# Optimization experiments

Hardware: AMD Instinct MI355X
Metric: run time of the kernel (lower is better)

## Reference

```python
import jax, jax.numpy as jnp
import numpy as np

B, S, D, H = 2, 2048, 1024, 16
HD = D // H

def setup_inputs() -> dict:
    key = jax.random.key(0)
    ks = jax.random.split(key, 5)
    s = 1.0 / np.sqrt(D)
    return {
        "x": jax.random.normal(ks[0], (B, S, D), dtype=jnp.float32),
        "Wq": jax.random.normal(ks[1], (D, D), dtype=jnp.float32) * s,
        "Wk": jax.random.normal(ks[2], (D, D), dtype=jnp.float32) * s,
        "Wv": jax.random.normal(ks[3], (D, D), dtype=jnp.float32) * s,
        "Wo": jax.random.normal(ks[4], (D, D), dtype=jnp.float32) * s,
        "bo": jnp.zeros((D,), dtype=jnp.float32),
    }

def reference(x, Wq, Wk, Wv, Wo, bo):
    b, n, _ = x.shape
    # QKV projections (no bias), reshape to [B, H, S, HD]
    def proj(W):
        return (x @ W.T).reshape(b, n, H, HD).transpose(0, 2, 1, 3)
    q, k, v = proj(Wq), proj(Wk), proj(Wv)
    scores = jnp.einsum("bhqd,bhkd->bhqk", q, k)
    causal = jnp.triu(jnp.ones((n, n), dtype=bool), k=1)
    scores = jnp.where(causal, -jnp.inf, scores)
    attn = jax.nn.softmax(scores / np.sqrt(HD), axis=-1)  # dropout p=0.0 (eval)
    ctx = jnp.einsum("bhqk,bhkd->bhqd", attn, v)
    ctx = ctx.transpose(0, 2, 1, 3).reshape(b, n, D)
    return ctx @ Wo.T + bo
```

## Files before the change

### kernel.cpp

```cpp
#include <hip/hip_runtime.h>
#include <stdint.h>


typedef __bf16 bf16_t;
typedef __bf16 bf16x8 __attribute__((ext_vector_type(8)));
typedef float  f32x4  __attribute__((ext_vector_type(4)));
typedef uint32_t u32x4 __attribute__((ext_vector_type(4)));

#define MFMA16(A, B, C) __builtin_amdgcn_mfma_f32_16x16x32_bf16(A, B, C, 0, 0, 0)

__device__ __forceinline__ void async_ld16(const bf16_t* g, bf16_t* l) {
  __builtin_amdgcn_global_load_lds(
      (const __attribute__((address_space(1))) void*)g,
      (__attribute__((address_space(3))) void*)l, 16, 0, 0);
}

__device__ __forceinline__ u32x4 ld8(const float* p) {
  const float4 a = *(const float4*)p;
  const float4 b = *(const float4*)(p + 4);
  union { u32x4 v; bf16_t h[8]; } r;
  r.h[0] = (bf16_t)a.x; r.h[1] = (bf16_t)a.y;
  r.h[2] = (bf16_t)a.z; r.h[3] = (bf16_t)a.w;
  r.h[4] = (bf16_t)b.x; r.h[5] = (bf16_t)b.y;
  r.h[6] = (bf16_t)b.z; r.h[7] = (bf16_t)b.w;
  return r.v;
}

__global__ __launch_bounds__(256) void cvt_all(
    const float* __restrict__ sx, const float* __restrict__ s1,
    const float* __restrict__ s2, const float* __restrict__ s3,
    bf16_t* __restrict__ dx, bf16_t* __restrict__ d1,
    bf16_t* __restrict__ d2, bf16_t* __restrict__ d3) {
  const int y = blockIdx.y;
  if (y != 0 && blockIdx.x >= 1024) return;
  const int i4 = (blockIdx.x * 256 + threadIdx.x) * 4;
  const float* s = (y == 0) ? sx : (y == 1) ? s1 : (y == 2) ? s2 : s3;
  bf16_t*      d = (y == 0) ? dx : (y == 1) ? d1 : (y == 2) ? d2 : d3;
  const float4 v = *(const float4*)(s + i4);
  union { uint64_t u; bf16_t h[4]; } pk;
  pk.h[0] = (bf16_t)v.x; pk.h[1] = (bf16_t)v.y;
  pk.h[2] = (bf16_t)v.z; pk.h[3] = (bf16_t)v.w;
  *(uint64_t*)(d + i4) = pk.u;
}

__global__ __launch_bounds__(256, 2) void gemm_qkv_a(
    const bf16_t* __restrict__ X,  const bf16_t* __restrict__ Wq,
    const bf16_t* __restrict__ Wk, const bf16_t* __restrict__ Wv,
    bf16_t* __restrict__ Q, bf16_t* __restrict__ K, bf16_t* __restrict__ V) {
  const int z = blockIdx.z;
  const bf16_t* W = (z == 0) ? Wq : (z == 1) ? Wk : Wv;
  bf16_t*       D = (z == 0) ? Q  : (z == 1) ? K  : V;
  const int mode = (z == 2) ? 1 : 0;

  __shared__ __align__(16) bf16_t As[128 * 64];
  __shared__ __align__(16) bf16_t Bs[128 * 64];

  const int tid  = threadIdx.x;
  const int lane = tid & 63;
  const int w    = tid >> 6;
  const int quad = lane >> 4;
  const int l15  = lane & 15;
  const int bm   = blockIdx.y * 128;
  const int bn   = blockIdx.x * 128;
  const int wm   = (w >> 1) * 64;
  const int wn   = (w & 1) * 64;
  const int sr   = lane >> 3;
  const int sc   = lane & 7;

  f32x4 acc[4][4] = {};

  for (int k0 = 0; k0 < 1024; k0 += 64) {
#pragma unroll
    for (int j = 0; j < 4; ++j) {
      const int r0 = w * 32 + j * 8;
      const int r  = r0 + sr;
      const int c  = sc ^ (r & 7);
      async_ld16(X + (size_t)(bm + r) * 1024 + k0 + c * 8, &As[r0 * 64]);
      async_ld16(W + (size_t)(bn + r) * 1024 + k0 + c * 8, &Bs[r0 * 64]);
    }
    __syncthreads();
#pragma unroll
    for (int kk = 0; kk < 64; kk += 32) {
      const int ck = (kk >> 3) + quad;
      bf16x8 aF[4], bF[4];
#pragma unroll
      for (int mt = 0; mt < 4; ++mt) {
        const int r = wm + mt * 16 + l15;
        aF[mt] = *(const bf16x8*)&As[r * 64 + (ck ^ (r & 7)) * 8];
      }
#pragma unroll
      for (int nt = 0; nt < 4; ++nt) {
        const int r = wn + nt * 16 + l15;
        bF[nt] = *(const bf16x8*)&Bs[r * 64 + (ck ^ (r & 7)) * 8];
      }
#pragma unroll
      for (int mt = 0; mt < 4; ++mt)
#pragma unroll
        for (int nt = 0; nt < 4; ++nt)
          acc[mt][nt] = MFMA16(aF[mt], bF[nt], acc[mt][nt]);
    }
    __syncthreads();
  }

#pragma unroll
  for (int mt = 0; mt < 4; ++mt) {
#pragma unroll
    for (int nt = 0; nt < 4; ++nt) {
      const int n  = bn + wn + nt * 16 + l15;
      const int mb = bm + wm + mt * 16 + quad * 4;
      const int h = n >> 6, hd = n & 63;
      if (mode == 0) {
#pragma unroll
        for (int r = 0; r < 4; ++r) {
          const int m = mb + r;
          const int b = m >> 11, s = m & 2047;
          D[(size_t)b * 2097152 + (size_t)h * 131072 + (size_t)s * 64 + hd] =
              (bf16_t)acc[mt][nt][r];
        }
      } else {
        const int b = mb >> 11, s0 = mb & 2047;
        union { uint64_t u; bf16_t h4[4]; } pk;
#pragma unroll
        for (int r = 0; r < 4; ++r) pk.h4[r] = (bf16_t)acc[mt][nt][r];
        *(uint64_t*)(D + (size_t)b * 2097152 + (size_t)h * 131072 +
                     (size_t)hd * 2048 + s0) = pk.u;
      }
    }
  }
}

__global__ __launch_bounds__(256, 2) void gemm_out_m(
    const bf16_t* __restrict__ ctx, const float* __restrict__ Wo,
    float* __restrict__ out, const float* __restrict__ bo) {
  __shared__ __align__(16) bf16_t As[64 * 64];
  __shared__ __align__(16) bf16_t Bs[128 * 64];

  const int tid  = threadIdx.x;
  const int lane = tid & 63;
  const int w    = tid >> 6;
  const int quad = lane >> 4;
  const int l15  = lane & 15;
  const int bm   = blockIdx.y * 64;
  const int bn   = blockIdx.x * 128;
  const int wm   = (w >> 1) * 32;
  const int wn   = (w & 1) * 64;
  const int sr   = lane >> 3;
  const int sc   = lane & 7;
  const int srow = tid >> 3;
  const int schk = tid & 7;

  f32x4 acc[2][4] = {};

  for (int k0 = 0; k0 < 1024; k0 += 64) {
#pragma unroll
    for (int j = 0; j < 2; ++j) {
      const int r0 = w * 16 + j * 8;
      const int r  = r0 + sr;
      const int c  = sc ^ (r & 7);
      async_ld16(ctx + (size_t)(bm + r) * 1024 + k0 + c * 8, &As[r0 * 64]);
    }
    u32x4 rb[4];
#pragma unroll
    for (int s2 = 0; s2 < 4; ++s2) {
      const int r = srow + s2 * 32;
      rb[s2] = ld8(Wo + (size_t)(bn + r) * 1024 + k0 + schk * 8);
    }
#pragma unroll
    for (int s2 = 0; s2 < 4; ++s2) {
      const int r = srow + s2 * 32;
      *(u32x4*)&Bs[r * 64 + ((schk ^ (r & 7)) * 8)] = rb[s2];
    }
    __syncthreads();
#pragma unroll
    for (int kk = 0; kk < 64; kk += 32) {
      const int ck = (kk >> 3) + quad;
      bf16x8 aF[2], bF[4];
#pragma unroll
      for (int mt = 0; mt < 2; ++mt) {
        const int r = wm + mt * 16 + l15;
        aF[mt] = *(const bf16x8*)&As[r * 64 + (ck ^ (r & 7)) * 8];
      }
#pragma unroll
      for (int nt = 0; nt < 4; ++nt) {
        const int r = wn + nt * 16 + l15;
        bF[nt] = *(const bf16x8*)&Bs[r * 64 + (ck ^ (r & 7)) * 8];
      }
#pragma unroll
      for (int mt = 0; mt < 2; ++mt)
#pragma unroll
        for (int nt = 0; nt < 4; ++nt)
          acc[mt][nt] = MFMA16(aF[mt], bF[nt], acc[mt][nt]);
    }
    __syncthreads();
  }

#pragma unroll
  for (int mt = 0; mt < 2; ++mt) {
#pragma unroll
    for (int nt = 0; nt < 4; ++nt) {
      const int n  = bn + wn + nt * 16 + l15;
      const int mb = bm + wm + mt * 16 + quad * 4;
      const float bv = bo[n];
#pragma unroll
      for (int r = 0; r < 4; ++r)
        out[(size_t)(mb + r) * 1024 + n] = acc[mt][nt][r] + bv;
    }
  }
}

__global__ __launch_bounds__(256, 2) void attn(
    const bf16_t* __restrict__ Qw, const bf16_t* __restrict__ Kw,
    const bf16_t* __restrict__ Vw, bf16_t* __restrict__ ctx) {
  constexpr int LDK = 72, LDV = 136, LDP = 136;
  __shared__ __align__(16) bf16_t Ks[128 * LDK];
  __shared__ __align__(16) bf16_t Vts[64 * LDV];
  __shared__ __align__(16) bf16_t Ps[128 * LDP];

  const int tid  = threadIdx.x;
  const int lane = tid & 63;
  const int w    = tid >> 6;
  const int quad = lane >> 4;
  const int l15  = lane & 15;
  const int b    = blockIdx.z;
  const int qt   = (b == 0) ? blockIdx.x : 15 - blockIdx.x;
  const int h    = blockIdx.y;
  const size_t bh = (size_t)(b * 16 + h) * (size_t)(2048 * 64);
  const bf16_t* Qh = Qw + bh;
  const bf16_t* Kh = Kw + bh;
  const bf16_t* Vh = Vw + bh;

  const int srow = tid >> 3, schk = tid & 7;
  const int vrow = tid >> 4, vchk = tid & 15;

  bf16_t* Qs = Ps;
  {
    u32x4 rq[4];
#pragma unroll
    for (int s2 = 0; s2 < 4; ++s2)
      rq[s2] = *(const u32x4*)(Qh + (size_t)(qt * 128 + srow + s2 * 32) * 64 + schk * 8);
#pragma unroll
    for (int s2 = 0; s2 < 4; ++s2)
      *(u32x4*)&Qs[(srow + s2 * 32) * LDK + schk * 8] = rq[s2];
  }
  __syncthreads();
  bf16x8 qF[2][2];
#pragma unroll
  for (int kq = 0; kq < 2; ++kq)
#pragma unroll
    for (int k2 = 0; k2 < 2; ++k2)
      qF[kq][k2] = *(const bf16x8*)
          &Qs[(w * 32 + kq * 16 + l15) * LDK + k2 * 32 + quad * 8];

  f32x4 O[2][4] = {};
  float mrow[2] = {-1e30f, -1e30f};
  float lrow[2] = {0.f, 0.f};

  const float sc_log2 = 0.125f * 1.44269504088896340736f;

  u32x4 rk[4], rv[4];
#pragma unroll
  for (int s2 = 0; s2 < 4; ++s2)
    rk[s2] = *(const u32x4*)(Kh + (size_t)(srow + s2 * 32) * 64 + schk * 8);
#pragma unroll
  for (int s2 = 0; s2 < 4; ++s2)
    rv[s2] = *(const u32x4*)(Vh + (size_t)(vrow + s2 * 16) * 2048 + vchk * 8);

  for (int kt = 0; kt <= qt; ++kt) {
    __syncthreads();
#pragma unroll
    for (int s2 = 0; s2 < 4; ++s2)
      *(u32x4*)&Ks[(srow + s2 * 32) * LDK + schk * 8] = rk[s2];
#pragma unroll
    for (int s2 = 0; s2 < 4; ++s2)
      *(u32x4*)&Vts[(vrow + s2 * 16) * LDV + vchk * 8] = rv[s2];
    __syncthreads();

    if (kt < qt) {
      const int kn = kt + 1;
#pragma unroll
      for (int s2 = 0; s2 < 4; ++s2)
        rk[s2] = *(const u32x4*)(Kh + (size_t)(kn * 128 + srow + s2 * 32) * 64 + schk * 8);
#pragma unroll
      for (int s2 = 0; s2 < 4; ++s2)
        rv[s2] = *(const u32x4*)(Vh + (size_t)(vrow + s2 * 16) * 2048 + kn * 128 + vchk * 8);
    }

    f32x4 St[2][8] = {};
#pragma unroll
    for (int ntk = 0; ntk < 8; ++ntk) {
      const int kr = ntk * 16 + l15;
#pragma unroll
      for (int k2 = 0; k2 < 2; ++k2) {
        const bf16x8 kF = *(const bf16x8*)&Ks[kr * LDK + k2 * 32 + quad * 8];
#pragma unroll
        for (int kq = 0; kq < 2; ++kq)
          St[kq][ntk] = MFMA16(kF, qF[kq][k2], St[kq][ntk]);
      }
    }

    if (kt == qt) {
#pragma unroll
      for (int kq = 0; kq < 2; ++kq) {
        const int ql = w * 32 + kq * 16 + l15;
#pragma unroll
        for (int ntk = 0; ntk < 8; ++ntk)
#pragma unroll
          for (int r = 0; r < 4; ++r)
            if (ntk * 16 + quad * 4 + r > ql) St[kq][ntk][r] = -1e30f;
      }
    }

    float aq[2];
#pragma unroll
    for (int kq = 0; kq < 2; ++kq) {
      float mx = -1e30f;
#pragma unroll
      for (int ntk = 0; ntk < 8; ++ntk)
#pragma unroll
        for (int r = 0; r < 4; ++r) mx = fmaxf(mx, St[kq][ntk][r]);
      mx = fmaxf(mx, __shfl_xor(mx, 16));
      mx = fmaxf(mx, __shfl_xor(mx, 32));
      const float mnew  = fmaxf(mrow[kq], mx);
      const float alpha = exp2f((mrow[kq] - mnew) * sc_log2);
      mrow[kq] = mnew;
      float rs = 0.f;
#pragma unroll
      for (int ntk = 0; ntk < 8; ++ntk) {
        union { uint64_t u; bf16_t h4[4]; } pk;
#pragma unroll
        for (int r = 0; r < 4; ++r) {
          const float p = exp2f((St[kq][ntk][r] - mnew) * sc_log2);
          rs += p;
          pk.h4[r] = (bf16_t)p;
        }
        *(uint64_t*)&Ps[(w * 32 + kq * 16 + l15) * LDP + ntk * 16 + quad * 4] = pk.u;
      }
      rs += __shfl_xor(rs, 16);
      rs += __shfl_xor(rs, 32);
      lrow[kq] = lrow[kq] * alpha + rs;
      aq[kq] = alpha;
    }

#pragma unroll
    for (int mt = 0; mt < 2; ++mt) {
#pragma unroll
      for (int r = 0; r < 4; ++r) {
        const float a = __shfl(aq[mt], quad * 4 + r);
#pragma unroll
        for (int nt = 0; nt < 4; ++nt) O[mt][nt][r] *= a;
      }
    }

#pragma unroll
    for (int kk = 0; kk < 128; kk += 32) {
      const int co = kk + quad * 8;
      bf16x8 pF[2], vF[4];
#pragma unroll
      for (int mt = 0; mt < 2; ++mt)
        pF[mt] = *(const bf16x8*)&Ps[(w * 32 + mt * 16 + l15) * LDP + co];
#pragma unroll
      for (int nt = 0; nt < 4; ++nt)
        vF[nt] = *(const bf16x8*)&Vts[(nt * 16 + l15) * LDV + co];
#pragma unroll
      for (int mt = 0; mt < 2; ++mt)
#pragma unroll
        for (int nt = 0; nt < 4; ++nt)
          O[mt][nt] = MFMA16(pF[mt], vF[nt], O[mt][nt]);
    }
  }

#pragma unroll
  for (int mt = 0; mt < 2; ++mt) {
#pragma unroll
    for (int r = 0; r < 4; ++r) {
      const float lr = __shfl(lrow[mt], quad * 4 + r);
      const float iv = 1.f / lr;
      const int s = qt * 128 + w * 32 + mt * 16 + quad * 4 + r;
#pragma unroll
      for (int nt = 0; nt < 4; ++nt) {
        const int hd = nt * 16 + l15;
        ctx[(size_t)(b * 2048 + s) * 1024 + h * 64 + hd] =
            (bf16_t)(O[mt][nt][r] * iv);
      }
    }
  }
}

extern "C" void kernel_launch(void* const* d_in, const int* in_sizes, int n_in,
                              void* d_out, int out_size, void* d_ws, size_t ws_size,
                              hipStream_t stream) {
  const float* x  = (const float*)d_in[0];
  const float* Wq = (const float*)d_in[1];
  const float* Wk = (const float*)d_in[2];
  const float* Wv = (const float*)d_in[3];
  const float* Wo = (const float*)d_in[4];
  const float* bo = (const float*)d_in[5];

  bf16_t* ws   = (bf16_t*)d_ws;
  bf16_t* Qw   = ws;
  bf16_t* Kw   = ws + 4194304;
  bf16_t* Vw   = ws + 8388608;
  bf16_t* ctxw = ws + 12582912;

  bf16_t* dscr = (bf16_t*)d_out;
  bf16_t* xb   = dscr;
  bf16_t* Wqb  = dscr + 4194304;
  bf16_t* Wkb  = dscr + 5242880;
  bf16_t* Wvb  = dscr + 6291456;
  float*  out  = (float*)d_out;

  dim3 blk(256);
  cvt_all<<<dim3(4096, 4), blk, 0, stream>>>(x, Wq, Wk, Wv, xb, Wqb, Wkb, Wvb);
  gemm_qkv_a<<<dim3(8, 32, 3), blk, 0, stream>>>(xb, Wqb, Wkb, Wvb, Qw, Kw, Vw);
  attn<<<dim3(16, 16, 2), blk, 0, stream>>>(Qw, Kw, Vw, ctxw);
  gemm_out_m<<<dim3(8, 64), blk, 0, stream>>>(ctxw, Wo, out, bo);
}
```

Before: 188.5 us.

## Double-buffer K/V via async global-to-LDS loads with XOR swizzle, chunk P through LDS

Result: slower. 194.3 us (+3.1%).

```diff
diff --git a/kernel.cpp b/kernel.cpp
--- a/kernel.cpp
+++ b/kernel.cpp
@@ -211,10 +211,9 @@
 __global__ __launch_bounds__(256, 2) void attn(
     const bf16_t* __restrict__ Qw, const bf16_t* __restrict__ Kw,
     const bf16_t* __restrict__ Vw, bf16_t* __restrict__ ctx) {
-  constexpr int LDK = 72, LDV = 136, LDP = 136;
-  __shared__ __align__(16) bf16_t Ks[128 * LDK];
-  __shared__ __align__(16) bf16_t Vts[64 * LDV];
-  __shared__ __align__(16) bf16_t Ps[128 * LDP];
+  __shared__ __align__(16) bf16_t Kb[2][128 * 64];
+  __shared__ __align__(16) bf16_t Vb[2][64 * 128];
+  __shared__ __align__(16) bf16_t Ps[128 * 40];
 
   const int tid  = threadIdx.x;
   const int lane = tid & 63;
@@ -230,60 +229,57 @@
   const bf16_t* Vh = Vw + bh;
 
   const int srow = tid >> 3, schk = tid & 7;
-  const int vrow = tid >> 4, vchk = tid & 15;
-
-  bf16_t* Qs = Ps;
+
+  auto stage_async = [&](int kt, int bi) {
+#pragma unroll
+    for (int j = 0; j < 4; ++j) {
+      const int r0 = w * 32 + j * 8;
+      const int r  = r0 + (lane >> 3);
+      const int c  = (lane & 7) ^ (r & 7);
+      async_ld16(Kh + (size_t)(kt * 128 + r) * 64 + c * 8, &Kb[bi][r0 * 64]);
+    }
+#pragma unroll
+    for (int j = 0; j < 4; ++j) {
+      const int r0 = w * 16 + j * 4;
+      const int hd = r0 + quad;
+      const int c  = (lane & 15) ^ (hd & 15);
+      async_ld16(Vh + (size_t)hd * 2048 + kt * 128 + c * 8, &Vb[bi][r0 * 128]);
+    }
+  };
+
+  stage_async(0, 1);
   {
     u32x4 rq[4];
 #pragma unroll
     for (int s2 = 0; s2 < 4; ++s2)
       rq[s2] = *(const u32x4*)(Qh + (size_t)(qt * 128 + srow + s2 * 32) * 64 + schk * 8);
 #pragma unroll
-    for (int s2 = 0; s2 < 4; ++s2)
-      *(u32x4*)&Qs[(srow + s2 * 32) * LDK + schk * 8] = rq[s2];
+    for (int s2 = 0; s2 < 4; ++s2) {
+      const int r = srow + s2 * 32;
+      *(u32x4*)&Kb[0][r * 64 + ((schk ^ (r & 7)) * 8)] = rq[s2];
+    }
   }
   __syncthreads();
   bf16x8 qF[2][2];
 #pragma unroll
   for (int kq = 0; kq < 2; ++kq)
 #pragma unroll
-    for (int k2 = 0; k2 < 2; ++k2)
-      qF[kq][k2] = *(const bf16x8*)
-          &Qs[(w * 32 + kq * 16 + l15) * LDK + k2 * 32 + quad * 8];
+    for (int k2 = 0; k2 < 2; ++k2) {
+      const int r  = w * 32 + kq * 16 + l15;
+      const int ck = k2 * 4 + quad;
+      qF[kq][k2] = *(const bf16x8*)&Kb[0][r * 64 + ((ck ^ (r & 7)) * 8)];
+    }
 
   f32x4 O[2][4] = {};
   float mrow[2] = {-1e30f, -1e30f};
   float lrow[2] = {0.f, 0.f};
-
   const float sc_log2 = 0.125f * 1.44269504088896340736f;
-
-  u32x4 rk[4], rv[4];
-#pragma unroll
-  for (int s2 = 0; s2 < 4; ++s2)
-    rk[s2] = *(const u32x4*)(Kh + (size_t)(srow + s2 * 32) * 64 + schk * 8);
-#pragma unroll
-  for (int s2 = 0; s2 < 4; ++s2)
-    rv[s2] = *(const u32x4*)(Vh + (size_t)(vrow + s2 * 16) * 2048 + vchk * 8);
 
   for (int kt = 0; kt <= qt; ++kt) {
     __syncthreads();
-#pragma unroll
-    for (int s2 = 0; s2 < 4; ++s2)
-      *(u32x4*)&Ks[(srow + s2 * 32) * LDK + schk * 8] = rk[s2];
-#pragma unroll
-    for (int s2 = 0; s2 < 4; ++s2)
-      *(u32x4*)&Vts[(vrow + s2 * 16) * LDV + vchk * 8] = rv[s2];
-    __syncthreads();
-
-    if (kt < qt) {
-      const int kn = kt + 1;
-#pragma unroll
-      for (int s2 = 0; s2 < 4; ++s2)
-        rk[s2] = *(const u32x4*)(Kh + (size_t)(kn * 128 + srow + s2 * 32) * 64 + schk * 8);
-#pragma unroll
-      for (int s2 = 0; s2 < 4; ++s2)
-        rv[s2] = *(const u32x4*)(Vh + (size_t)(vrow + s2 * 16) * 2048 + kn * 128 + vchk * 8);
-    }
+    if (kt < qt) stage_async(kt + 1, kt & 1);
+    const bf16_t* K_ = Kb[(kt + 1) & 1];
+    const bf16_t* V_ = Vb[(kt + 1) & 1];
 
     f32x4 St[2][8] = {};
 #pragma unroll
@@ -291,7 +287,8 @@
       const int kr = ntk * 16 + l15;
 #pragma unroll
       for (int k2 = 0; k2 < 2; ++k2) {
-        const bf16x8 kF = *(const bf16x8*)&Ks[kr * LDK + k2 * 32 + quad * 8];
+        const int ck = k2 * 4 + quad;
+        const bf16x8 kF = *(const bf16x8*)&K_[kr * 64 + ((ck ^ (kr & 7)) * 8)];
 #pragma unroll
         for (int kq = 0; kq < 2; ++kq)
           St[kq][ntk] = MFMA16(kF, qF[kq][k2], St[kq][ntk]);
@@ -310,7 +307,7 @@
       }
     }
 
-    float aq[2];
+    float aq[2], mn[2], rs[2] = {0.f, 0.f};
 #pragma unroll
     for (int kq = 0; kq < 2; ++kq) {
       float mx = -1e30f;
@@ -320,27 +317,10 @@
         for (int r = 0; r < 4; ++r) mx = fmaxf(mx, St[kq][ntk][r]);
       mx = fmaxf(mx, __shfl_xor(mx, 16));
       mx = fmaxf(mx, __shfl_xor(mx, 32));
-      const float mnew  = fmaxf(mrow[kq], mx);
-      const float alpha = exp2f((mrow[kq] - mnew) * sc_log2);
-      mrow[kq] = mnew;
-      float rs = 0.f;
-#pragma unroll
-      for (int ntk = 0; ntk < 8; ++ntk) {
-        union { uint64_t u; bf16_t h4[4]; } pk;
-#pragma unroll
-        for (int r = 0; r < 4; ++r) {
-          const float p = exp2f((St[kq][ntk][r] - mnew) * sc_log2);
-          rs += p;
-          pk.h4[r] = (bf16_t)p;
-        }
-        *(uint64_t*)&Ps[(w * 32 + kq * 16 + l15) * LDP + ntk * 16 + quad * 4] = pk.u;
-      }
-      rs += __shfl_xor(rs, 16);
-      rs += __shfl_xor(rs, 32);
-      lrow[kq] = lrow[kq] * alpha + rs;
-      aq[kq] = alpha;
-    }
-
+      mn[kq] = fmaxf(mrow[kq], mx);
+      aq[kq] = exp2f((mrow[kq] - mn[kq]) * sc_log2);
+      mrow[kq] = mn[kq];
+    }
 #pragma unroll
     for (int mt = 0; mt < 2; ++mt) {
 #pragma unroll
@@ -352,20 +332,46 @@
     }
 
 #pragma unroll
-    for (int kk = 0; kk < 128; kk += 32) {
-      const int co = kk + quad * 8;
+    for (int c = 0; c < 4; ++c) {
+#pragma unroll
+      for (int kq = 0; kq < 2; ++kq) {
+        const int q = w * 32 + kq * 16 + l15;
+#pragma unroll
+        for (int t = 0; t < 2; ++t) {
+          const int ntk = c * 2 + t;
+          union { uint64_t u; bf16_t h4[4]; } pk;
+#pragma unroll
+          for (int r = 0; r < 4; ++r) {
+            const float p = exp2f((St[kq][ntk][r] - mn[kq]) * sc_log2);
+            rs[kq] += p;
+            pk.h4[r] = (bf16_t)p;
+          }
+          *(uint64_t*)&Ps[q * 40 + t * 16 + quad * 4] = pk.u;
+        }
+      }
       bf16x8 pF[2], vF[4];
 #pragma unroll
       for (int mt = 0; mt < 2; ++mt)
-        pF[mt] = *(const bf16x8*)&Ps[(w * 32 + mt * 16 + l15) * LDP + co];
-#pragma unroll
-      for (int nt = 0; nt < 4; ++nt)
-        vF[nt] = *(const bf16x8*)&Vts[(nt * 16 + l15) * LDV + co];
+        pF[mt] = *(const bf16x8*)&Ps[(w * 32 + mt * 16 + l15) * 40 + quad * 8];
+#pragma unroll
+      for (int nt = 0; nt < 4; ++nt) {
+        const int hd = nt * 16 + l15;
+        const int lc = c * 4 + quad;
+        vF[nt] = *(const bf16x8*)&V_[hd * 128 + ((lc ^ (hd & 15)) * 8)];
+      }
 #pragma unroll
       for (int mt = 0; mt < 2; ++mt)
 #pragma unroll
         for (int nt = 0; nt < 4; ++nt)
           O[mt][nt] = MFMA16(pF[mt], vF[nt], O[mt][nt]);
+    }
+
+#pragma unroll
+    for (int kq = 0; kq < 2; ++kq) {
+      float r = rs[kq];
+      r += __shfl_xor(r, 16);
+      r += __shfl_xor(r, 32);
+      lrow[kq] = lrow[kq] * aq[kq] + r;
     }
   }
 
```
